# Optimization experiments

Hardware: AMD Instinct MI355X
Metric: run time of the kernel (lower is better)

The kernel has to match this reference:

```python
import jax, jax.numpy as jnp
import numpy as np

N = 100000      # nodes
E = 1600000     # edges (avg degree 16)
FEAT, HID, OUT = 128, 64, 40
P_DROP = 0.5


def setup_inputs() -> dict:
    key = jax.random.key(0)
    ks = jax.random.split(key, 7)
    x = jax.random.normal(ks[0], (N, FEAT), dtype=jnp.float32)
    edge_index = jax.random.randint(ks[1], (2, E), 0, N, dtype=jnp.int32)
    W1 = jax.random.normal(ks[2], (FEAT, HID), dtype=jnp.float32) / np.float32(np.sqrt(FEAT))
    b1 = jnp.zeros((HID,), jnp.float32)
    W2 = jax.random.normal(ks[3], (HID, OUT), dtype=jnp.float32) / np.float32(np.sqrt(HID))
    b2 = jnp.zeros((OUT,), jnp.float32)
    # scaled inverted-dropout mask: values in {0, 1/(1-p)}
    keep = jax.random.bernoulli(ks[4], 1.0 - P_DROP, (N, HID))
    drop_mask = keep.astype(jnp.float32) / np.float32(1.0 - P_DROP)
    return {"x": x, "edge_index": edge_index, "W1": W1, "b1": b1,
            "W2": W2, "b2": b2, "drop_mask": drop_mask}


def _gcn_conv(x, W, b, src, dst):
    """PyG GCNConv: h = xW; add self-loops; sym-normalized scatter-add; +b."""
    h = x @ W                                   # [N, D_out]
    ones = jnp.ones((src.shape[0],), h.dtype)
    deg = jax.ops.segment_sum(ones, dst, num_segments=N) + 1.0  # +1 self-loop
    dinv = jax.lax.rsqrt(deg)                   # deg > 0 due to self-loops
    norm = dinv[src] * dinv[dst]                # [E]
    msg = h[src] * norm[:, None]                # gather + scale
    agg = jax.ops.segment_sum(msg, dst, num_segments=N)
    agg = agg + h * (dinv * dinv)[:, None]      # self-loop contribution
    return agg + b


def reference(x, edge_index, W1, b1, W2, b2, drop_mask):
    src, dst = edge_index[0], edge_index[1]
    h = _gcn_conv(x, W1, b1, src, dst)
    h = jax.nn.relu(h)
    h = h * drop_mask                           # F.dropout (pre-drawn mask)
    out = _gcn_conv(h, W2, b2, src, dst)
    return out
```

## Files before the change

### kernel.cpp

```cpp
#include <hip/hip_runtime.h>
#include <hip/hip_fp16.h>

#define NN     100000
#define NE     1600000
#define FEAT   128
#define HID    64
#define OUTD   40
#define BSH    5
#define BNODES 32
#define NBKT   (NN / BNODES)
#define CAP    768
#define CCHUNK 2048
#define WSCALE 262144.0f
#define WINV   (1.0f / 262144.0f)

typedef _Float16 half8 __attribute__((ext_vector_type(8)));
typedef float    f32x4 __attribute__((ext_vector_type(4)));

__global__ __launch_bounds__(256) void k_pairs(const int* __restrict__ src,
                                               const int* __restrict__ dst,
                                               int* __restrict__ bfill,
                                               int* __restrict__ pairs) {
    __shared__ int bcnt[NBKT];
    __shared__ int gb[NBKT];
    int t = threadIdx.x;
    for (int i = t; i < NBKT; i += 256) bcnt[i] = 0;
    __syncthreads();
    int e0 = blockIdx.x * CCHUNK;
    int pk[8], bb[8], off[8];
    #pragma unroll
    for (int i = 0; i < 8; ++i) {
        int e = e0 + i * 256 + t;
        if (e < NE) {
            int d = dst[e];
            pk[i]  = (src[e] << 7) | (d & (BNODES - 1));
            bb[i]  = d >> BSH;
            off[i] = atomicAdd(&bcnt[bb[i]], 1);
        } else bb[i] = -1;
    }
    __syncthreads();
    for (int i = t; i < NBKT; i += 256) {
        int c = bcnt[i];
        gb[i] = c ? (i * CAP + atomicAdd(&bfill[i], c)) : 0;
    }
    __syncthreads();
    #pragma unroll
    for (int i = 0; i < 8; ++i)
        if (bb[i] >= 0) pairs[gb[bb[i]] + off[i]] = pk[i];
}

__global__ __launch_bounds__(256) void k_degdinv(const int* __restrict__ pairs,
                                                 const int* __restrict__ bfill,
                                                 float* __restrict__ dinv) {
    __shared__ int hist[BNODES];
    int b = blockIdx.x, t = threadIdx.x;
    if (t < BNODES) hist[t] = 0;
    __syncthreads();
    int base = b * CAP, count = bfill[b];
    for (int i = t; i < count; i += 256)
        atomicAdd(&hist[pairs[base + i] & (BNODES - 1)], 1);
    __syncthreads();
    if (t < BNODES) dinv[(b << BSH) + t] = rsqrtf((float)hist[t] + 1.0f);
}

__global__ __launch_bounds__(256) void k_csr(const int* __restrict__ pairs,
                                             int* __restrict__ bfill,
                                             int* __restrict__ csr) {
    __shared__ int hist[256];
    __shared__ int sc[256];
    int b = blockIdx.x, t = threadIdx.x;
    hist[t] = 0;
    __syncthreads();
    int base = b * CAP, count = bfill[b];
    for (int i = t; i < count; i += 256)
        atomicAdd(&hist[(pairs[base + i] >> 16) & 255], 1);
    __syncthreads();
    int v = hist[t];
    sc[t] = v;
    __syncthreads();
    for (int off = 1; off < 256; off <<= 1) {
        int u = (t >= off) ? sc[t - off] : 0;
        __syncthreads();
        sc[t] += u;
        __syncthreads();
    }
    hist[t] = sc[t] - v;
    __syncthreads();
    for (int i = t; i < count; i += 256) {
        int p = pairs[base + i];
        int pos = atomicAdd(&hist[(p >> 16) & 255], 1);
        csr[base + pos] = p;
    }
    int padded = (count + 31) & ~31;
    for (int i = count + t; i < padded; i += 256)
        csr[base + i] = (NN << 7);
    __syncthreads();
    if (t == 0) bfill[b] = padded;
}

__global__ __launch_bounds__(256) void k_maskbits(const float* __restrict__ mask,
                                                  unsigned long long* __restrict__ mb) {
    int node = blockIdx.x * 4 + (threadIdx.x >> 6);
    if (node >= NN) return;
    int l = threadIdx.x & 63;
    float m = mask[(size_t)node * HID + l];
    unsigned long long bits = __ballot(m != 0.f);
    if (l == 0) mb[node] = bits;
}

__global__ __launch_bounds__(256) void k_wprep(const float* __restrict__ W1,
                                               const float* __restrict__ W2,
                                               _Float16* __restrict__ w1f,
                                               _Float16* __restrict__ w2f,
                                               __half* __restrict__ h1s,
                                               __half* __restrict__ hhs) {
    int t = threadIdx.x;
    for (int it = t; it < 16 * 64; it += 256) {
        int f = it >> 6, l = it & 63;
        int kk = f >> 2, n = f & 3;
        int krow = kk * 32 + (l >> 4) * 8;
        int col  = n * 16 + (l & 15);
        #pragma unroll
        for (int i = 0; i < 8; ++i)
            w1f[it * 8 + i] = (_Float16)W1[(krow + i) * HID + col];
    }
    for (int it = t; it < 6 * 64; it += 256) {
        int f = it >> 6, l = it & 63;
        int kk = f / 3, n = f - kk * 3;
        int krow = kk * 32 + (l >> 4) * 8;
        int col  = n * 16 + (l & 15);
        #pragma unroll
        for (int i = 0; i < 8; ++i)
            w2f[it * 8 + i] = (col < OUTD) ? (_Float16)W2[(krow + i) * OUTD + col]
                                           : (_Float16)0.f;
    }
    if (t < HID) {
        h1s[(size_t)NN * HID + t] = __float2half(0.f);
        hhs[(size_t)NN * HID + t] = __float2half(0.f);
    }
}

__global__ __launch_bounds__(256) void k_mgemm1(const float* __restrict__ x,
                                                const _Float16* __restrict__ w1f,
                                                const float* __restrict__ dinv,
                                                __half* __restrict__ h1s) {
    int wid = (blockIdx.x * 256 + threadIdx.x) >> 6;
    int l = threadIdx.x & 63;
    if (wid >= NN / 16) return;
    half8 bf[4][4];
    #pragma unroll
    for (int kk = 0; kk < 4; ++kk)
        #pragma unroll
        for (int n = 0; n < 4; ++n)
            bf[kk][n] = ((const half8*)w1f)[(kk * 4 + n) * 64 + l];
    f32x4 acc[4] = {};
    int arow = wid * 16 + (l & 15);
    const float* xp = x + (size_t)arow * FEAT + (l >> 4) * 8;
    #pragma unroll
    for (int kk = 0; kk < 4; ++kk) {
        float4 u0 = *(const float4*)(xp + kk * 32);
        float4 u1 = *(const float4*)(xp + kk * 32 + 4);
        half8 af;
        af[0] = (_Float16)u0.x; af[1] = (_Float16)u0.y;
        af[2] = (_Float16)u0.z; af[3] = (_Float16)u0.w;
        af[4] = (_Float16)u1.x; af[5] = (_Float16)u1.y;
        af[6] = (_Float16)u1.z; af[7] = (_Float16)u1.w;
        #pragma unroll
        for (int n = 0; n < 4; ++n)
            acc[n] = __builtin_amdgcn_mfma_f32_16x16x32_f16(af, bf[kk][n], acc[n], 0, 0, 0);
    }
    int orow = wid * 16 + (l >> 4) * 4;
    int ocol = l & 15;
    float dv[4];
    #pragma unroll
    for (int r = 0; r < 4; ++r) dv[r] = dinv[orow + r];
    #pragma unroll
    for (int n = 0; n < 4; ++n)
        #pragma unroll
        for (int r = 0; r < 4; ++r)
            h1s[(size_t)(orow + r) * HID + n * 16 + ocol] = __float2half(acc[n][r] * dv[r]);
}

template<int MODE>
__global__ __launch_bounds__(256) void k_bagg(const int* __restrict__ csr,
                                              const int* __restrict__ bfill,
                                              const float* __restrict__ dinv,
                                              const __half* __restrict__ feat,
                                              const float* __restrict__ b1,
                                              const unsigned long long* __restrict__ maskbits,
                                              __half* __restrict__ outp) {
    __shared__ int acc[BNODES * HID];
    int t = threadIdx.x, wv = t >> 6, l = t & 63;
    int b = blockIdx.x;
    int4* a4 = (int4*)acc;
    for (int i = t; i < BNODES * HID / 4; i += 256) a4[i] = make_int4(0, 0, 0, 0);
    __syncthreads();
    int base = b * CAP;
    int count = bfill[b];
    const char* fb = (const char*)feat + ((size_t)l * 2);
    for (int j = wv * 8; j < count; j += 32) {
        int e0 = csr[base + j + 0], e1 = csr[base + j + 1];
        int e2 = csr[base + j + 2], e3 = csr[base + j + 3];
        int e4 = csr[base + j + 4], e5 = csr[base + j + 5];
        int e6 = csr[base + j + 6], e7 = csr[base + j + 7];
        float a0 = __half2float(*(const __half*)(fb + (unsigned)(e0 & ~127)));
        float a1 = __half2float(*(const __half*)(fb + (unsigned)(e1 & ~127)));
        float a2 = __half2float(*(const __half*)(fb + (unsigned)(e2 & ~127)));
        float a3 = __half2float(*(const __half*)(fb + (unsigned)(e3 & ~127)));
        float a4v = __half2float(*(const __half*)(fb + (unsigned)(e4 & ~127)));
        float a5 = __half2float(*(const __half*)(fb + (unsigned)(e5 & ~127)));
        float a6 = __half2float(*(const __half*)(fb + (unsigned)(e6 & ~127)));
        float a7 = __half2float(*(const __half*)(fb + (unsigned)(e7 & ~127)));
        atomicAdd(&acc[((e0 & 31) << 6) + l], (int)(a0 * WSCALE));
        atomicAdd(&acc[((e1 & 31) << 6) + l], (int)(a1 * WSCALE));
        atomicAdd(&acc[((e2 & 31) << 6) + l], (int)(a2 * WSCALE));
        atomicAdd(&acc[((e3 & 31) << 6) + l], (int)(a3 * WSCALE));
        atomicAdd(&acc[((e4 & 31) << 6) + l], (int)(a4v * WSCALE));
        atomicAdd(&acc[((e5 & 31) << 6) + l], (int)(a5 * WSCALE));
        atomicAdd(&acc[((e6 & 31) << 6) + l], (int)(a6 * WSCALE));
        atomicAdd(&acc[((e7 & 31) << 6) + l], (int)(a7 * WSCALE));
    }
    __syncthreads();
    for (int n = wv; n < BNODES; n += 4) {
        int node = (b << BSH) + n;
        float di = dinv[node];
        float selfv = __half2float(feat[(size_t)node * HID + l]);
        float vv = ((float)acc[(n << 6) + l] * WINV + selfv) * di;
        if (MODE == 0) {
            vv += b1[l];
            vv = vv > 0.f ? vv : 0.f;
            unsigned long long mb = maskbits[node];
            vv = ((mb >> l) & 1ull) ? vv * 2.0f * di : 0.0f;
        }
        outp[(size_t)node * HID + l] = __float2half(vv);
    }
}

__global__ __launch_bounds__(256) void k_mgemm2(const __half* __restrict__ aggh,
                                                const _Float16* __restrict__ w2f,
                                                const float* __restrict__ b2,
                                                float* __restrict__ out) {
    int wid = (blockIdx.x * 256 + threadIdx.x) >> 6;
    int l = threadIdx.x & 63;
    if (wid >= NN / 16) return;
    half8 bf[2][3];
    #pragma unroll
    for (int kk = 0; kk < 2; ++kk)
        #pragma unroll
        for (int n = 0; n < 3; ++n)
            bf[kk][n] = ((const half8*)w2f)[(kk * 3 + n) * 64 + l];
    f32x4 acc[3] = {};
    int arow = wid * 16 + (l & 15);
    const _Float16* hp = (const _Float16*)aggh + (size_t)arow * HID + (l >> 4) * 8;
    #pragma unroll
    for (int kk = 0; kk < 2; ++kk) {
        half8 af = *(const half8*)(hp + kk * 32);
        #pragma unroll
        for (int n = 0; n < 3; ++n)
            acc[n] = __builtin_amdgcn_mfma_f32_16x16x32_f16(af, bf[kk][n], acc[n], 0, 0, 0);
    }
    int orow = wid * 16 + (l >> 4) * 4;
    int ocol = l & 15;
    #pragma unroll
    for (int n = 0; n < 3; ++n) {
        int col = n * 16 + ocol;
        if (col < OUTD) {
            float bb = b2[col];
            #pragma unroll
            for (int r = 0; r < 4; ++r)
                out[(size_t)(orow + r) * OUTD + col] = acc[n][r] + bb;
        }
    }
}

extern "C" void kernel_launch(void* const* d_in, const int* in_sizes, int n_in,
                              void* d_out, int out_size, void* d_ws, size_t ws_size,
                              hipStream_t stream) {
    const float* x    = (const float*)d_in[0];
    const int*   ei   = (const int*)d_in[1];
    const int*   src  = ei;
    const int*   dst  = ei + NE;
    const float* W1   = (const float*)d_in[2];
    const float* b1   = (const float*)d_in[3];
    const float* W2   = (const float*)d_in[4];
    const float* b2   = (const float*)d_in[5];
    const float* mask = (const float*)d_in[6];
    float* out = (float*)d_out;

    char* ws = (char*)d_ws;
    int*      bfill = (int*)ws;            ws += (size_t)NBKT * 4;
    float*    dinv  = (float*)ws;          ws += (size_t)NN * 4;
    unsigned long long* maskb = (unsigned long long*)ws; ws += (size_t)NN * 8;
    _Float16* w1f   = (_Float16*)ws;       ws += 16 * 64 * 8 * 2;
    _Float16* w2f   = (_Float16*)ws;       ws += 6 * 64 * 8 * 2;
    int*      csr   = (int*)ws;            ws += (size_t)NBKT * CAP * 4;
    __half*   h1s   = (__half*)ws;         ws += (size_t)(NN + 1) * HID * 2;
    __half*   hhs   = (__half*)ws;         ws += (size_t)(NN + 1) * HID * 2;
    int*      pairs = (int*)hhs;
    __half*   aggh  = h1s;

    hipMemsetAsync(bfill, 0, (size_t)NBKT * 4, stream);

    k_pairs   <<<(NE + CCHUNK - 1) / CCHUNK, 256, 0, stream>>>(src, dst, bfill, pairs);
    k_degdinv <<<NBKT, 256, 0, stream>>>(pairs, bfill, dinv);
    k_csr     <<<NBKT, 256, 0, stream>>>(pairs, bfill, csr);
    k_maskbits<<<(NN + 3) / 4, 256, 0, stream>>>(mask, maskb);
    k_wprep   <<<1, 256, 0, stream>>>(W1, W2, w1f, w2f, h1s, hhs);

    k_mgemm1  <<<(NN / 16 + 3) / 4, 256, 0, stream>>>(x, w1f, dinv, h1s);
    k_bagg<0> <<<NBKT, 256, 0, stream>>>(csr, bfill, dinv, h1s, b1, maskb, hhs);
    k_bagg<1> <<<NBKT, 256, 0, stream>>>(csr, bfill, dinv, hhs, nullptr, nullptr, aggh);
    k_mgemm2  <<<(NN / 16 + 3) / 4, 256, 0, stream>>>(aggh, w2f, b2, out);
}
```

Baseline: 195.9 us.

## Bucket edges into 256-node superbuckets and sub-sort per 32-node aggregation block

Edge binning in k_pairs now uses 256-node superbuckets, which cuts the number of global bucket counters and shared histogram entries. k_csr builds a two-level key (32-node sub-bucket, source range) and emits eight padded sub-segments per superbucket, recording their start and length for the aggregation kernels. Larger, fuller buckets are meant to lower atomic contention and scatter overhead in the preprocessing kernels. In exchange k_csr uses more shared memory and does more scan work, and CAP now assumes a superbucket never holds more than 5120 edges.

```diff
diff --git a/kernel.cpp b/kernel.cpp
--- a/kernel.cpp
+++ b/kernel.cpp
@@ -6,10 +6,10 @@
 #define FEAT   128
 #define HID    64
 #define OUTD   40
-#define BSH    5
 #define BNODES 32
-#define NBKT   (NN / BNODES)
-#define CAP    768
+#define NSB    ((NN + 255) / 256)
+#define NBAGG  (NSB * 8)
+#define CAP    5120
 #define CCHUNK 2048
 #define WSCALE 262144.0f
 #define WINV   (1.0f / 262144.0f)
@@ -21,10 +21,10 @@
                                                const int* __restrict__ dst,
                                                int* __restrict__ bfill,
                                                int* __restrict__ pairs) {
-    __shared__ int bcnt[NBKT];
-    __shared__ int gb[NBKT];
+    __shared__ int bcnt[NSB];
+    __shared__ int gb[NSB];
     int t = threadIdx.x;
-    for (int i = t; i < NBKT; i += 256) bcnt[i] = 0;
+    for (int i = t; i < NSB; i += 256) bcnt[i] = 0;
     __syncthreads();
     int e0 = blockIdx.x * CCHUNK;
     int pk[8], bb[8], off[8];
@@ -33,13 +33,13 @@
         int e = e0 + i * 256 + t;
         if (e < NE) {
             int d = dst[e];
-            pk[i]  = (src[e] << 7) | (d & (BNODES - 1));
-            bb[i]  = d >> BSH;
+            pk[i]  = (src[e] << 8) | (d & 255);
+            bb[i]  = d >> 8;
             off[i] = atomicAdd(&bcnt[bb[i]], 1);
         } else bb[i] = -1;
     }
     __syncthreads();
-    for (int i = t; i < NBKT; i += 256) {
+    for (int i = t; i < NSB; i += 256) {
         int c = bcnt[i];
         gb[i] = c ? (i * CAP + atomicAdd(&bfill[i], c)) : 0;
     }
@@ -52,50 +52,89 @@
 __global__ __launch_bounds__(256) void k_degdinv(const int* __restrict__ pairs,
                                                  const int* __restrict__ bfill,
                                                  float* __restrict__ dinv) {
-    __shared__ int hist[BNODES];
+    __shared__ int hist[256];
     int b = blockIdx.x, t = threadIdx.x;
-    if (t < BNODES) hist[t] = 0;
+    hist[t] = 0;
     __syncthreads();
     int base = b * CAP, count = bfill[b];
     for (int i = t; i < count; i += 256)
-        atomicAdd(&hist[pairs[base + i] & (BNODES - 1)], 1);
-    __syncthreads();
-    if (t < BNODES) dinv[(b << BSH) + t] = rsqrtf((float)hist[t] + 1.0f);
+        atomicAdd(&hist[pairs[base + i] & 255], 1);
+    __syncthreads();
+    int node = (b << 8) + t;
+    if (node < NN) dinv[node] = rsqrtf((float)hist[t] + 1.0f);
 }
 
 __global__ __launch_bounds__(256) void k_csr(const int* __restrict__ pairs,
-                                             int* __restrict__ bfill,
+                                             const int* __restrict__ bfill,
+                                             int* __restrict__ sb_beg,
+                                             int* __restrict__ sb_cnt,
                                              int* __restrict__ csr) {
-    __shared__ int hist[256];
-    __shared__ int sc[256];
+    __shared__ int hist[2048];
+    __shared__ int exs[2048];
+    __shared__ int part[256];
+    __shared__ int poff[9];
+    __shared__ int sstart[8];
+    __shared__ int dtot[8];
     int b = blockIdx.x, t = threadIdx.x;
-    hist[t] = 0;
+    #pragma unroll
+    for (int k = 0; k < 8; ++k) hist[t * 8 + k] = 0;
     __syncthreads();
     int base = b * CAP, count = bfill[b];
-    for (int i = t; i < count; i += 256)
-        atomicAdd(&hist[(pairs[base + i] >> 16) & 255], 1);
-    __syncthreads();
-    int v = hist[t];
-    sc[t] = v;
-    __syncthreads();
-    for (int off = 1; off < 256; off <<= 1) {
-        int u = (t >= off) ? sc[t - off] : 0;
-        __syncthreads();
-        sc[t] += u;
-        __syncthreads();
-    }
-    hist[t] = sc[t] - v;
-    __syncthreads();
     for (int i = t; i < count; i += 256) {
         int p = pairs[base + i];
-        int pos = atomicAdd(&hist[(p >> 16) & 255], 1);
-        csr[base + pos] = p;
-    }
-    int padded = (count + 31) & ~31;
-    for (int i = count + t; i < padded; i += 256)
-        csr[base + i] = (NN << 7);
-    __syncthreads();
-    if (t == 0) bfill[b] = padded;
+        int key = (((p & 255) >> 5) << 8) | ((p >> 17) & 255);
+        atomicAdd(&hist[key], 1);
+    }
+    __syncthreads();
+    int loc[8], s0 = 0;
+    #pragma unroll
+    for (int k = 0; k < 8; ++k) { loc[k] = s0; s0 += hist[t * 8 + k]; }
+    part[t] = s0;
+    __syncthreads();
+    for (int off = 1; off < 256; off <<= 1) {
+        int u = (t >= off) ? part[t - off] : 0;
+        __syncthreads();
+        part[t] += u;
+        __syncthreads();
+    }
+    int pex = part[t] - s0;
+    #pragma unroll
+    for (int k = 0; k < 8; ++k) exs[t * 8 + k] = pex + loc[k];
+    __syncthreads();
+    if (t < 8) {
+        sstart[t] = exs[t * 256];
+        int end = (t == 7) ? count : exs[(t + 1) * 256];
+        dtot[t] = end - sstart[t];
+    }
+    __syncthreads();
+    if (t == 0) {
+        poff[0] = 0;
+        for (int d = 0; d < 8; ++d) poff[d + 1] = poff[d] + ((dtot[d] + 31) & ~31);
+    }
+    __syncthreads();
+    #pragma unroll
+    for (int k = 0; k < 8; ++k) {
+        int key = t * 8 + k;
+        int d = key >> 8;
+        exs[key] = poff[d] + (exs[key] - sstart[d]);
+        hist[key] = 0;
+    }
+    __syncthreads();
+    for (int i = t; i < count; i += 256) {
+        int p = pairs[base + i];
+        int key = (((p & 255) >> 5) << 8) | ((p >> 17) & 255);
+        int pos = exs[key] + atomicAdd(&hist[key], 1);
+        csr[base + pos] = ((p >> 8) << 7) | (p & 31);
+    }
+    for (int d = 0; d < 8; ++d) {
+        int padded = (dtot[d] + 31) & ~31;
+        for (int i = dtot[d] + t; i < padded; i += 256)
+            csr[base + poff[d] + i] = (NN << 7);
+    }
+    if (t < 8) {
+        sb_beg[b * 8 + t] = base + poff[t];
+        sb_cnt[b * 8 + t] = (dtot[t] + 31) & ~31;
+    }
 }
 
 __global__ __launch_bounds__(256) void k_maskbits(const float* __restrict__ mask,
@@ -183,7 +222,8 @@
 
 template<int MODE>
 __global__ __launch_bounds__(256) void k_bagg(const int* __restrict__ csr,
-                                              const int* __restrict__ bfill,
+                                              const int* __restrict__ sb_beg,
+                                              const int* __restrict__ sb_cnt,
                                               const float* __restrict__ dinv,
                                               const __half* __restrict__ feat,
                                               const float* __restrict__ b1,
@@ -191,12 +231,13 @@
                                               __half* __restrict__ outp) {
     __shared__ int acc[BNODES * HID];
     int t = threadIdx.x, wv = t >> 6, l = t & 63;
-    int b = blockIdx.x;
+    int bb = blockIdx.x;
     int4* a4 = (int4*)acc;
     for (int i = t; i < BNODES * HID / 4; i += 256) a4[i] = make_int4(0, 0, 0, 0);
     __syncthreads();
-    int base = b * CAP;
-    int count = bfill[b];
+    int base  = sb_beg[bb];
+    int count = sb_cnt[bb];
+    int node0 = (bb >> 3) * 256 + (bb & 7) * 32;
     const char* fb = (const char*)feat + ((size_t)l * 2);
     for (int j = wv * 8; j < count; j += 32) {
         int e0 = csr[base + j + 0], e1 = csr[base + j + 1];
@@ -222,7 +263,8 @@
     }
     __syncthreads();
     for (int n = wv; n < BNODES; n += 4) {
-        int node = (b << BSH) + n;
+        int node = node0 + n;
+        if (node >= NN) break;
         float di = dinv[node];
         float selfv = __half2float(feat[(size_t)node * HID + l]);
         float vv = ((float)acc[(n << 6) + l] * WINV + selfv) * di;
@@ -288,27 +330,29 @@
     float* out = (float*)d_out;
 
     char* ws = (char*)d_ws;
-    int*      bfill = (int*)ws;            ws += (size_t)NBKT * 4;
-    float*    dinv  = (float*)ws;          ws += (size_t)NN * 4;
+    int*      bfill  = (int*)ws;           ws += (size_t)NSB * 4;
+    int*      sb_beg = (int*)ws;           ws += (size_t)NBAGG * 4;
+    int*      sb_cnt = (int*)ws;           ws += (size_t)NBAGG * 4;
+    float*    dinv   = (float*)ws;         ws += (size_t)NN * 4;
     unsigned long long* maskb = (unsigned long long*)ws; ws += (size_t)NN * 8;
-    _Float16* w1f   = (_Float16*)ws;       ws += 16 * 64 * 8 * 2;
-    _Float16* w2f   = (_Float16*)ws;       ws += 6 * 64 * 8 * 2;
-    int*      csr   = (int*)ws;            ws += (size_t)NBKT * CAP * 4;
-    __half*   h1s   = (__half*)ws;         ws += (size_t)(NN + 1) * HID * 2;
-    __half*   hhs   = (__half*)ws;         ws += (size_t)(NN + 1) * HID * 2;
-    int*      pairs = (int*)hhs;
-    __half*   aggh  = h1s;
-
-    hipMemsetAsync(bfill, 0, (size_t)NBKT * 4, stream);
+    _Float16* w1f    = (_Float16*)ws;      ws += 16 * 64 * 8 * 2;
+    _Float16* w2f    = (_Float16*)ws;      ws += 6 * 64 * 8 * 2;
+    int*      csr    = (int*)ws;           ws += (size_t)NSB * CAP * 4;
+    __half*   h1s    = (__half*)ws;        ws += (size_t)(NN + 1) * HID * 2;
+    __half*   hhs    = (__half*)ws;        ws += (size_t)(NN + 1) * HID * 2;
+    int*      pairs  = (int*)hhs;
+    __half*   aggh   = h1s;
+
+    hipMemsetAsync(bfill, 0, (size_t)NSB * 4, stream);
 
     k_pairs   <<<(NE + CCHUNK - 1) / CCHUNK, 256, 0, stream>>>(src, dst, bfill, pairs);
-    k_degdinv <<<NBKT, 256, 0, stream>>>(pairs, bfill, dinv);
-    k_csr     <<<NBKT, 256, 0, stream>>>(pairs, bfill, csr);
+    k_degdinv <<<NSB, 256, 0, stream>>>(pairs, bfill, dinv);
+    k_csr     <<<NSB, 256, 0, stream>>>(pairs, bfill, sb_beg, sb_cnt, csr);
     k_maskbits<<<(NN + 3) / 4, 256, 0, stream>>>(mask, maskb);
     k_wprep   <<<1, 256, 0, stream>>>(W1, W2, w1f, w2f, h1s, hhs);
 
     k_mgemm1  <<<(NN / 16 + 3) / 4, 256, 0, stream>>>(x, w1f, dinv, h1s);
-    k_bagg<0> <<<NBKT, 256, 0, stream>>>(csr, bfill, dinv, h1s, b1, maskb, hhs);
-    k_bagg<1> <<<NBKT, 256, 0, stream>>>(csr, bfill, dinv, hhs, nullptr, nullptr, aggh);
+    k_bagg<0> <<<NBAGG, 256, 0, stream>>>(csr, sb_beg, sb_cnt, dinv, h1s, b1, maskb, hhs);
+    k_bagg<1> <<<NBAGG, 256, 0, stream>>>(csr, sb_beg, sb_cnt, dinv, hhs, nullptr, nullptr, aggh);
     k_mgemm2  <<<(NN / 16 + 3) / 4, 256, 0, stream>>>(aggh, w2f, b2, out);
 }
```

After: 181.5 us. 7.4% less time.
